# Performance work log

Hardware: AMD Instinct MI355X
Metric: run time of the kernel (lower is better)

The kernel has to match this reference:

```python
import jax, jax.numpy as jnp
import numpy as np

NU, NI, E, B, D = 100000, 50000, 1000000, 250000, 64
MSG_EPS = 1e-7   # GENConv message epsilon
BN_EPS = 1e-5    # BatchNorm1d epsilon


def setup_inputs() -> dict:
    key = jax.random.key(0)
    ks = jax.random.split(key, 8)
    x_user = jax.random.normal(ks[0], (NU, D), jnp.float32)
    x_item = jax.random.normal(ks[1], (NI, D), jnp.float32)
    src_u = jax.random.randint(ks[2], (E,), 0, NU)
    dst_i = jax.random.randint(ks[3], (E,), 0, NI)
    edge_ui = jnp.stack([src_u, dst_i]).astype(jnp.int32)   # (user, rates, item)
    pu = jax.random.randint(ks[4], (B,), 0, NU)
    pi = jax.random.randint(ks[5], (B,), 0, NI)
    pred_edge = jnp.stack([pu, pi]).astype(jnp.int32)       # supervision edges
    # per-layer (3), per-edge-type (2: 0 = user->item conv, 1 = item->user conv)
    W1 = jax.random.normal(ks[6], (3, 2, D, 2 * D), jnp.float32) / np.sqrt(D).astype(np.float32)
    b1 = jnp.zeros((3, 2, 2 * D), jnp.float32)
    gamma = jnp.ones((3, 2, 2 * D), jnp.float32)
    beta = jnp.zeros((3, 2, 2 * D), jnp.float32)
    W2 = jax.random.normal(ks[7], (3, 2, 2 * D, D), jnp.float32) / np.sqrt(2 * D).astype(np.float32)
    b2 = jnp.zeros((3, 2, D), jnp.float32)
    return dict(x_user=x_user, x_item=x_item, W1=W1, b1=b1, gamma=gamma,
                beta=beta, W2=W2, b2=b2, edge_ui=edge_ui, pred_edge=pred_edge)


def _genconv(x_src, x_dst, src_idx, dst_idx, n_dst, W1, b1, g, bt, W2, b2):
    # message: relu(x_j) + eps   (no edge attrs)
    m = jax.nn.relu(x_src[src_idx]) + MSG_EPS                     # [E, D]
    # softmax aggregation over incoming edges per destination (t = 1)
    mx = jax.ops.segment_max(m, dst_idx, num_segments=n_dst)      # [N_dst, D]
    ex = jnp.exp(m - mx[dst_idx])
    den = jax.ops.segment_sum(ex, dst_idx, num_segments=n_dst)
    w = ex / den[dst_idx]
    agg = jax.ops.segment_sum(w * m, dst_idx, num_segments=n_dst) # [N_dst, D]
    # root skip + MLP([D, 2D, D]) with BatchNorm + ReLU on hidden layer
    h = agg + x_dst
    h = h @ W1 + b1                                               # [N_dst, 2D]
    mu = h.mean(axis=0)
    var = h.var(axis=0)
    h = g * (h - mu) * jax.lax.rsqrt(var + BN_EPS) + bt
    h = jax.nn.relu(h)
    return h @ W2 + b2                                            # [N_dst, D]


def reference(x_user, x_item, W1, b1, gamma, beta, W2, b2, edge_ui, pred_edge):
    u_idx, i_idx = edge_ui[0], edge_ui[1]
    xu, xi = x_user, x_item
    for l in range(3):
        # to_hetero: one conv per edge type; aggr='sum' trivial (one edge type per dst)
        new_i = _genconv(xu, xi, u_idx, i_idx, NI,
                         W1[l, 0], b1[l, 0], gamma[l, 0], beta[l, 0], W2[l, 0], b2[l, 0])
        new_u = _genconv(xi, xu, i_idx, u_idx, NU,
                         W1[l, 1], b1[l, 1], gamma[l, 1], beta[l, 1], W2[l, 1], b2[l, 1])
        xu = jax.nn.relu(new_u)
        xi = jax.nn.relu(new_i)
    # decoder: dot product on supervision edges
    return (xu[pred_edge[0]] * xi[pred_edge[1]]).sum(axis=-1)     # [B]
```

## Files before the change

### kernel.cpp

```cpp
#include <hip/hip_runtime.h>
#include <hip/hip_fp16.h>

#define NUSR 100000
#define NITM 50000
#define NEDG 1000000
#define NPRED 250000
#define DD 64
#define DD2 128
#define MSG_EPS 1e-7f
#define BN_EPS 1e-5f
#define SCAN_B 1024

#define KI 98
#define KU 98
#define EPB 4096
#define ICAP 1536

typedef _Float16 f16x8 __attribute__((ext_vector_type(8)));
typedef float f32x4 __attribute__((ext_vector_type(4)));


__global__ __launch_bounds__(256) void count_k(
    const int* __restrict__ u_idx, const int* __restrict__ i_idx,
    int* __restrict__ deg_u, int* __restrict__ deg_i)
{
    int base = (blockIdx.x * 256 + threadIdx.x) * 4;
    int u[4], it[4];
    #pragma unroll
    for (int q = 0; q < 4; q++) {
        int e = base + q;
        u[q]  = (e < NEDG) ? u_idx[e] : -1;
        it[q] = (e < NEDG) ? i_idx[e] : -1;
    }
    #pragma unroll
    for (int q = 0; q < 4; q++) if (it[q] >= 0) atomicAdd(&deg_i[it[q]], 1);
    #pragma unroll
    for (int q = 0; q < 4; q++) if (u[q] >= 0) atomicAdd(&deg_u[u[q]], 1);
}

__global__ __launch_bounds__(SCAN_B) void scan1_k(
    const int* __restrict__ deg_i, const int* __restrict__ deg_u,
    int* __restrict__ part_i, int* __restrict__ part_u,
    int* __restrict__ bsum_i, int* __restrict__ bsum_u, int nbi)
{
    __shared__ int s[SCAN_B];
    const int* deg; int* partial; int* bsum; int n, bb;
    if ((int)blockIdx.x < nbi) { deg = deg_i; partial = part_i; bsum = bsum_i; n = NITM; bb = blockIdx.x; }
    else { deg = deg_u; partial = part_u; bsum = bsum_u; n = NUSR; bb = blockIdx.x - nbi; }
    int tid = threadIdx.x;
    int i = bb * SCAN_B + tid;
    s[tid] = (i < n) ? deg[i] : 0;
    __syncthreads();
    for (int off = 1; off < SCAN_B; off <<= 1) {
        int t = (tid >= off) ? s[tid - off] : 0;
        __syncthreads();
        s[tid] += t;
        __syncthreads();
    }
    if (i < n) partial[i] = s[tid];
    if (tid == SCAN_B - 1) bsum[bb] = s[tid];
}

__global__ __launch_bounds__(128) void scan2_k(
    int* __restrict__ bsum_i, int* __restrict__ bsum_u, int nbi, int nbu)
{
    __shared__ int s[128];
    int* bsum = (blockIdx.x == 0) ? bsum_i : bsum_u;
    int nb = (blockIdx.x == 0) ? nbi : nbu;
    int tid = threadIdx.x;
    s[tid] = (tid < nb) ? bsum[tid] : 0;
    __syncthreads();
    for (int off = 1; off < 128; off <<= 1) {
        int t = (tid >= off) ? s[tid - off] : 0;
        __syncthreads();
        s[tid] += t;
        __syncthreads();
    }
    if (tid < nb) bsum[tid] = (tid == 0) ? 0 : s[tid - 1];
}

__global__ __launch_bounds__(SCAN_B) void scan3_k(
    const int* __restrict__ deg_i, const int* __restrict__ deg_u,
    const int* __restrict__ part_i, const int* __restrict__ part_u,
    const int* __restrict__ bsum_i, const int* __restrict__ bsum_u,
    int* __restrict__ rowptr_i, int* __restrict__ rowptr_u,
    int* __restrict__ bcur_i, int* __restrict__ bcur_u, int nbi)
{
    const int* deg; const int* partial; const int* bsum;
    int* rowptr; int* bcur; int n, bb, sh;
    if ((int)blockIdx.x < nbi) {
        deg = deg_i; partial = part_i; bsum = bsum_i;
        rowptr = rowptr_i; bcur = bcur_i; n = NITM; bb = blockIdx.x; sh = 9;
    } else {
        deg = deg_u; partial = part_u; bsum = bsum_u;
        rowptr = rowptr_u; bcur = bcur_u; n = NUSR; bb = blockIdx.x - nbi; sh = 10;
    }
    int i = bb * SCAN_B + threadIdx.x;
    if (i < n) {
        int rs = partial[i] - deg[i] + bsum[bb];
        rowptr[i] = rs;
        if ((i & ((1 << sh) - 1)) == 0) bcur[i >> sh] = rs;
    }
    if (i == 0) rowptr[n] = NEDG;
}

__global__ __launch_bounds__(256) void part_k(
    const int* __restrict__ u_idx, const int* __restrict__ i_idx,
    int* __restrict__ bcur_i, int* __restrict__ bcur_u,
    int* __restrict__ pair_i, int* __restrict__ pair_u)
{
    __shared__ int lh_i[KI], lh_u[KU];
    __shared__ int lb_i[KI], lb_u[KU];
    int tid = threadIdx.x;
    int base = blockIdx.x * EPB;
    int u[16], it[16];
    #pragma unroll
    for (int q = 0; q < 16; q++) {
        int e = base + q * 256 + tid;
        u[q]  = (e < NEDG) ? u_idx[e] : -1;
        it[q] = (e < NEDG) ? i_idx[e] : -1;
    }
    if (tid < KI) lh_i[tid] = 0;
    if (tid >= 128 && tid < 128 + KU) lh_u[tid - 128] = 0;
    __syncthreads();
    #pragma unroll
    for (int q = 0; q < 16; q++) if (it[q] >= 0) {
        atomicAdd(&lh_i[it[q] >> 9], 1);
        atomicAdd(&lh_u[u[q] >> 10], 1);
    }
    __syncthreads();
    if (tid < KI) { int c = lh_i[tid]; lb_i[tid] = c ? atomicAdd(&bcur_i[tid], c) : 0; }
    if (tid >= 128 && tid < 128 + KU) {
        int k = tid - 128; int c = lh_u[k];
        lb_u[k] = c ? atomicAdd(&bcur_u[k], c) : 0;
    }
    __syncthreads();
    #pragma unroll
    for (int q = 0; q < 16; q++) if (it[q] >= 0) {
        int pi_ = atomicAdd(&lb_i[it[q] >> 9], 1);
        pair_i[pi_] = ((it[q] & 511) << 17) | u[q];
        int pu_ = atomicAdd(&lb_u[u[q] >> 10], 1);
        pair_u[pu_] = ((u[q] & 1023) << 16) | it[q];
    }
}

__global__ __launch_bounds__(1024) void bscat_k(
    const int* __restrict__ pair_i, const int* __restrict__ pair_u,
    const int* __restrict__ rowptr_i, const int* __restrict__ rowptr_u,
    int* __restrict__ csr_i, int* __restrict__ csr_u)
{
    __shared__ int cur[1024];
    int b = blockIdx.x;
    const int* pair; const int* rowptr; int* csr;
    int base_row, wrows, n, shsrc;
    if (b < KI) {
        pair = pair_i; rowptr = rowptr_i; csr = csr_i;
        base_row = b << 9; wrows = 512; n = NITM; shsrc = 17;
    } else {
        int k = b - KI;
        pair = pair_u; rowptr = rowptr_u; csr = csr_u;
        base_row = k << 10; wrows = 1024; n = NUSR; shsrc = 16;
    }
    int nrows = min(wrows, n - base_row);
    int t = threadIdx.x;
    if (t < nrows) cur[t] = rowptr[base_row + t];
    __syncthreads();
    int bstart = rowptr[base_row];
    int bend = rowptr[min(base_row + wrows, n)];
    int srcmask = (1 << shsrc) - 1;
    for (int e = bstart + t; e < bend; e += 1024) {
        int v = pair[e];
        int pos = atomicAdd(&cur[v >> shsrc], 1);
        csr[pos] = v & srcmask;
    }
}

__global__ __launch_bounds__(256) void msg0_k(
    const float* __restrict__ xu, const float* __restrict__ xi,
    __half* __restrict__ msg_u, __half* __restrict__ msg_i)
{
    int i = blockIdx.x * 256 + threadIdx.x;
    const float* x; __half* msg; int idx;
    if (i < NUSR * 16) { x = xu; msg = msg_u; idx = i; }
    else { int j = i - NUSR * 16; if (j >= NITM * 16) return; x = xi; msg = msg_i; idx = j; }
    float4 v = ((const float4*)x)[idx];
    __half2 a = __floats2half2_rn(fmaxf(v.x, 0.f) + MSG_EPS, fmaxf(v.y, 0.f) + MSG_EPS);
    __half2 b = __floats2half2_rn(fmaxf(v.z, 0.f) + MSG_EPS, fmaxf(v.w, 0.f) + MSG_EPS);
    ((__half2*)msg)[idx * 2]     = a;
    ((__half2*)msg)[idx * 2 + 1] = b;
}

__global__ __launch_bounds__(256) void wconv_k(
    const float* __restrict__ W1, const float* __restrict__ W2,
    __half* __restrict__ W1t, __half* __restrict__ W2t)
{
    int idx = blockIdx.x * 256 + threadIdx.x;
    if (idx >= 6 * 8192) return;
    int m = idx >> 13, rem = idx & 8191;
    {
        int k = rem >> 7, c = rem & 127;
        W1t[m * 8192 + c * 64 + k] = __float2half(W1[idx]);
    }
    {
        int k = rem >> 6, c = rem & 63;
        W2t[m * 8192 + c * 128 + k] = __float2half(W2[idx]);
    }
}

#define UPD4(U) { \
    float2 va=__half22float2(*(__half2*)&(U).x); \
    float2 vb=__half22float2(*(__half2*)&(U).y); \
    float2 vc=__half22float2(*(__half2*)&(U).z); \
    float2 vd=__half22float2(*(__half2*)&(U).w); \
    float e0=__expf(va.x), e1=__expf(va.y), e2=__expf(vb.x), e3=__expf(vb.y); \
    float e4=__expf(vc.x), e5=__expf(vc.y), e6=__expf(vd.x), e7=__expf(vd.y); \
    d0+=e0; n0=fmaf(e0,va.x,n0); d1+=e1; n1=fmaf(e1,va.y,n1); \
    d2+=e2; n2=fmaf(e2,vb.x,n2); d3+=e3; n3=fmaf(e3,vb.y,n3); \
    d4+=e4; n4=fmaf(e4,vc.x,n4); d5+=e5; n5=fmaf(e5,vc.y,n5); \
    d6+=e6; n6=fmaf(e6,vd.x,n6); d7+=e7; n7=fmaf(e7,vd.y,n7); }

#define GBODY(IDXE) { \
    int j = beg; \
    for (; j + 4 <= end; j += 4) { \
        int s0=(IDXE(j)), s1=(IDXE(j+1)), s2=(IDXE(j+2)), s3=(IDXE(j+3)); \
        uint4 u0 = mp4[s0*8+l8]; uint4 u1 = mp4[s1*8+l8]; \
        uint4 u2 = mp4[s2*8+l8]; uint4 u3 = mp4[s3*8+l8]; \
        UPD4(u0) UPD4(u1) UPD4(u2) UPD4(u3) } \
    for (; j < end; j++) { int ss=(IDXE(j)); uint4 uu = mp4[ss*8+l8]; UPD4(uu) } }

#define IDX_L(jj) su.idx[(jj)]
#define IDX_G(jj) csr[blkBeg + (jj)]

union AggSU { int idx[ICAP]; float red[8][128]; };

__global__ __launch_bounds__(256) void aggemm1f_k(
    const __half* __restrict__ msg_i_src, const __half* __restrict__ msg_u_src,
    const float* __restrict__ xi_cur, const float* __restrict__ xu_cur,
    const int* __restrict__ rowptr_i, const int* __restrict__ rowptr_u,
    const int* __restrict__ csr_i, const int* __restrict__ csr_u,
    const __half* __restrict__ W1t_l,
    const float* __restrict__ b1_l,
    __half* __restrict__ h1_i, __half* __restrict__ h1_u,
    double* __restrict__ gs_l,
    int gI)
{
    __shared__ _Float16 sA[64][88];
    __shared__ AggSU su;

    int side = ((int)blockIdx.x < gI) ? 0 : 1;
    int bb = side ? (blockIdx.x - gI) : blockIdx.x;
    const __half* msg = side ? msg_i_src : msg_u_src;
    const float* xdst = side ? xu_cur : xi_cur;
    const int* rowptr = side ? rowptr_u : rowptr_i;
    const int* csr    = side ? csr_u : csr_i;
    const __half* W1t = W1t_l + (size_t)side * 8192;
    const float* b1   = b1_l + side * DD2;
    __half* h1        = side ? h1_u : h1_i;
    double* gsum      = gs_l + side * 256;
    double* gsq       = gsum + 128;
    int N             = side ? NUSR : NITM;

    int t = threadIdx.x;
    int r0 = bb * 64;
    int w = t >> 6, lane = t & 63;
    int g = lane >> 3, l8 = lane & 7;
    int q = lane >> 4, ln = lane & 15;
    const uint4* mp4 = (const uint4*)msg;

    int blkBeg = rowptr[r0];
    int blkEnd = rowptr[min(r0 + 64, N)];
    int nE = blkEnd - blkBeg;
    for (int e = t; e < nE && e < ICAP; e += 256) su.idx[e] = csr[blkBeg + e];
    __syncthreads();

    #pragma unroll
    for (int ii = 0; ii < 2; ii++) {
        int rr = w * 16 + ii * 8 + g;
        int r = r0 + rr;
        uint4 o = make_uint4(0u, 0u, 0u, 0u);
        if (r < N) {
            int beg = rowptr[r] - blkBeg;
            int end = rowptr[r + 1] - blkBeg;
            float d0=0.f,d1=0.f,d2=0.f,d3=0.f,d4=0.f,d5=0.f,d6=0.f,d7=0.f;
            float n0=0.f,n1=0.f,n2=0.f,n3=0.f,n4=0.f,n5=0.f,n6=0.f,n7=0.f;
            if (end <= ICAP) { GBODY(IDX_L) } else { GBODY(IDX_G) }
            bool nz = end > beg;
            float a0 = nz ? n0/d0 : 0.f, a1 = nz ? n1/d1 : 0.f;
            float a2 = nz ? n2/d2 : 0.f, a3 = nz ? n3/d3 : 0.f;
            float a4 = nz ? n4/d4 : 0.f, a5 = nz ? n5/d5 : 0.f;
            float a6 = nz ? n6/d6 : 0.f, a7 = nz ? n7/d7 : 0.f;
            const float4* xr = (const float4*)xdst + (size_t)r * 16;
            float4 x0 = xr[l8 * 2], x1 = xr[l8 * 2 + 1];
            __half2 p0 = __floats2half2_rn(a0 + x0.x, a1 + x0.y);
            __half2 p1 = __floats2half2_rn(a2 + x0.z, a3 + x0.w);
            __half2 p2 = __floats2half2_rn(a4 + x1.x, a5 + x1.y);
            __half2 p3 = __floats2half2_rn(a6 + x1.z, a7 + x1.w);
            o.x = *(unsigned int*)&p0; o.y = *(unsigned int*)&p1;
            o.z = *(unsigned int*)&p2; o.w = *(unsigned int*)&p3;
        }
        *(uint4*)&sA[rr][l8 * 8] = o;
    }
    __syncthreads();

    f16x8 afr[4][2], bfr[2][2];
    #pragma unroll
    for (int rt = 0; rt < 4; rt++)
        #pragma unroll
        for (int ks = 0; ks < 2; ks++)
            afr[rt][ks] = *(const f16x8*)&sA[rt * 16 + ln][ks * 32 + q * 8];
    const f16x8* Wv = (const f16x8*)W1t;
    #pragma unroll
    for (int ct = 0; ct < 2; ct++)
        #pragma unroll
        for (int ks = 0; ks < 2; ks++)
            bfr[ct][ks] = Wv[(w * 32 + ct * 16 + ln) * 8 + ks * 4 + q];

    f32x4 acc[4][2];
    #pragma unroll
    for (int rt = 0; rt < 4; rt++)
        #pragma unroll
        for (int ct = 0; ct < 2; ct++)
            acc[rt][ct] = (f32x4){0.f, 0.f, 0.f, 0.f};

    #pragma unroll
    for (int rt = 0; rt < 4; rt++)
        #pragma unroll
        for (int ct = 0; ct < 2; ct++) {
            acc[rt][ct] = __builtin_amdgcn_mfma_f32_16x16x32_f16(
                afr[rt][0], bfr[ct][0], acc[rt][ct], 0, 0, 0);
            acc[rt][ct] = __builtin_amdgcn_mfma_f32_16x16x32_f16(
                afr[rt][1], bfr[ct][1], acc[rt][ct], 0, 0, 0);
        }

    float b1c0 = b1[w * 32 + ln];
    float b1c1 = b1[w * 32 + 16 + ln];
    float ps0 = 0.f, pq0 = 0.f, ps1 = 0.f, pq1 = 0.f;
    #pragma unroll
    for (int rt = 0; rt < 4; rt++) {
        #pragma unroll
        for (int i = 0; i < 4; i++) {
            int r = r0 + rt * 16 + q * 4 + i;
            if (r < N) {
                float h0 = acc[rt][0][i] + b1c0;
                float h1v = acc[rt][1][i] + b1c1;
                h1[(size_t)r * DD2 + w * 32 + ln] = __float2half(h0);
                h1[(size_t)r * DD2 + w * 32 + 16 + ln] = __float2half(h1v);
                ps0 += h0; pq0 += h0 * h0;
                ps1 += h1v; pq1 += h1v * h1v;
            }
        }
    }
    su.red[q][w * 32 + ln] = ps0;      su.red[q][w * 32 + 16 + ln] = ps1;
    su.red[4 + q][w * 32 + ln] = pq0;  su.red[4 + q][w * 32 + 16 + ln] = pq1;
    __syncthreads();
    if (t < 128) {
        float s = 0.f, qq = 0.f;
        #pragma unroll
        for (int k = 0; k < 4; k++) { s += su.red[k][t]; qq += su.red[4 + k][t]; }
        atomicAdd(&gsum[t], (double)s);
        atomicAdd(&gsq[t],  (double)qq);
    }
}

__global__ __launch_bounds__(256) void gemm2f_k(
    const __half* __restrict__ h1_i, const __half* __restrict__ h1_u,
    const double* __restrict__ gs_l,
    const float* __restrict__ gamma_l, const float* __restrict__ beta_l,
    const __half* __restrict__ W2t_l, const float* __restrict__ b2_l,
    float* __restrict__ xi_new, float* __restrict__ xu_new,
    __half* __restrict__ msgi_out, __half* __restrict__ msgu_out, int gI)
{
    __shared__ _Float16 sA[64][136];
    __shared__ float2 sss[DD2];

    int side = ((int)blockIdx.x < gI) ? 0 : 1;
    int bb = side ? (blockIdx.x - gI) : blockIdx.x;
    const __half* h1   = side ? h1_u : h1_i;
    const double* gsum = gs_l + side * 256;
    const double* gsq  = gsum + 128;
    const float* gamma = gamma_l + side * DD2;
    const float* beta  = beta_l + side * DD2;
    const __half* W2t  = W2t_l + (size_t)side * 8192;
    const float* b2    = b2_l + side * DD;
    float* xnew        = side ? xu_new : xi_new;
    __half* msgout     = side ? msgu_out : msgi_out;
    int N              = side ? NUSR : NITM;

    int t = threadIdx.x;
    if (t < 128) {
        double mean = gsum[t] / (double)N;
        double var  = gsq[t] / (double)N - mean * mean;
        float inv = (float)(1.0 / sqrt(var + (double)BN_EPS));
        float sc = gamma[t] * inv;
        sss[t] = make_float2(sc, beta[t] - (float)mean * sc);
    }
    __syncthreads();

    int r0 = bb * 64;
    for (int i = t; i < 2048; i += 256) {
        int rr = i >> 5, c4 = i & 31;
        int r = r0 + rr;
        uint2 o = make_uint2(0u, 0u);
        if (r < N) {
            uint2 hv = ((const uint2*)h1)[(size_t)r * 32 + c4];
            float2 va = __half22float2(*(__half2*)&hv.x);
            float2 vb = __half22float2(*(__half2*)&hv.y);
            float2 s0 = sss[c4 * 4], s1 = sss[c4 * 4 + 1];
            float2 s2 = sss[c4 * 4 + 2], s3 = sss[c4 * 4 + 3];
            va.x = fmaxf(fmaf(va.x, s0.x, s0.y), 0.f);
            va.y = fmaxf(fmaf(va.y, s1.x, s1.y), 0.f);
            vb.x = fmaxf(fmaf(vb.x, s2.x, s2.y), 0.f);
            vb.y = fmaxf(fmaf(vb.y, s3.x, s3.y), 0.f);
            __half2 a = __floats2half2_rn(va.x, va.y);
            __half2 b = __floats2half2_rn(vb.x, vb.y);
            o.x = *(unsigned int*)&a; o.y = *(unsigned int*)&b;
        }
        *(uint2*)&sA[rr][c4 * 4] = o;
    }
    __syncthreads();

    int w = t >> 6, lane = t & 63, q = lane >> 4, ln = lane & 15;
    f32x4 acc[4];
    #pragma unroll
    for (int rt = 0; rt < 4; rt++) acc[rt] = (f32x4){0.f, 0.f, 0.f, 0.f};

    const f16x8* Wv = (const f16x8*)W2t;
    #pragma unroll
    for (int ks = 0; ks < 4; ks++) {
        f16x8 bf = Wv[(w * 16 + ln) * 16 + ks * 4 + q];
        #pragma unroll
        for (int rt = 0; rt < 4; rt++) {
            f16x8 af = *(const f16x8*)&sA[rt * 16 + ln][ks * 32 + q * 8];
            acc[rt] = __builtin_amdgcn_mfma_f32_16x16x32_f16(af, bf, acc[rt], 0, 0, 0);
        }
    }

    int c = w * 16 + ln;
    float bb2 = b2[c];
    #pragma unroll
    for (int rt = 0; rt < 4; rt++) {
        #pragma unroll
        for (int i = 0; i < 4; i++) {
            int r = r0 + rt * 16 + q * 4 + i;
            if (r < N) {
                float o = fmaxf(acc[rt][i] + bb2, 0.f);
                xnew[(size_t)r * DD + c] = o;
                msgout[(size_t)r * DD + c] = __float2half(o + MSG_EPS);
            }
        }
    }
}

__global__ __launch_bounds__(256) void decode_k(
    const float* __restrict__ xu, const float* __restrict__ xi,
    const int* __restrict__ pu, const int* __restrict__ pi,
    float* __restrict__ out)
{
    int idx = blockIdx.x * 256 + threadIdx.x;
    int b = idx >> 4, lane = idx & 15;
    if (b >= NPRED) return;
    int u = pu[b], it = pi[b];
    float4 a = ((const float4*)(xu + (size_t)u * DD))[lane];
    float4 c = ((const float4*)(xi + (size_t)it * DD))[lane];
    float s = a.x * c.x + a.y * c.y + a.z * c.z + a.w * c.w;
    #pragma unroll
    for (int off = 8; off; off >>= 1) s += __shfl_down(s, off, 16);
    if (lane == 0) out[b] = s;
}

extern "C" void kernel_launch(void* const* d_in, const int* in_sizes, int n_in,
                              void* d_out, int out_size, void* d_ws, size_t ws_size,
                              hipStream_t stream)
{
    const float* x_user = (const float*)d_in[0];
    const float* x_item = (const float*)d_in[1];
    const float* W1    = (const float*)d_in[2];
    const float* b1    = (const float*)d_in[3];
    const float* gamma = (const float*)d_in[4];
    const float* beta  = (const float*)d_in[5];
    const float* W2    = (const float*)d_in[6];
    const float* b2    = (const float*)d_in[7];
    const int* edge = (const int*)d_in[8];
    const int* pred = (const int*)d_in[9];
    float* out = (float*)d_out;

    const int* u_idx = edge;
    const int* i_idx = edge + NEDG;

    char* p = (char*)d_ws;
    #define ALLOC(ptr, type, count) \
        type* ptr = (type*)p; p += (((size_t)(count) * sizeof(type)) + 255) & ~(size_t)255;

    ALLOC(deg_i, int, NITM)
    ALLOC(deg_u, int, NUSR)
    ALLOC(gsumAll, double, 12 * 256)
    size_t zero_span = (char*)p - (char*)deg_i;
    ALLOC(part_i, int, NITM)
    ALLOC(part_u, int, NUSR)
    ALLOC(bsum_i, int, 128)
    ALLOC(bsum_u, int, 128)
    ALLOC(bcur_i, int, 128)
    ALLOC(bcur_u, int, 128)
    ALLOC(rowptr_i, int, NITM + 1)
    ALLOC(rowptr_u, int, NUSR + 1)
    ALLOC(csr_i, int, NEDG)
    ALLOC(csr_u, int, NEDG)
    ALLOC(h1_i, __half, (size_t)NITM * DD2)
    ALLOC(h1_u, __half, (size_t)NUSR * DD2)
    ALLOC(W1t, __half, 6 * 8192)
    ALLOC(W2t, __half, 6 * 8192)
    ALLOC(xu0, float, (size_t)NUSR * DD)
    ALLOC(xu1, float, (size_t)NUSR * DD)
    ALLOC(xi0, float, (size_t)NITM * DD)
    ALLOC(xi1, float, (size_t)NITM * DD)
    ALLOC(msg_u, __half, (size_t)NUSR * DD)
    ALLOC(msg_i0, __half, (size_t)NITM * DD)
    ALLOC(msg_i1, __half, (size_t)NITM * DD)
    #undef ALLOC
    float* xu_buf[2] = {xu0, xu1};
    float* xi_buf[2] = {xi0, xi1};

    int* pair_i = (int*)h1_i;
    int* pair_u = (int*)h1_u;

    hipMemsetAsync(deg_i, 0, zero_span, stream);
    int eb4 = (NEDG / 4 + 255) / 256;
    count_k<<<eb4, 256, 0, stream>>>(u_idx, i_idx, deg_u, deg_i);

    int nbi = (NITM + SCAN_B - 1) / SCAN_B;
    int nbu = (NUSR + SCAN_B - 1) / SCAN_B;
    scan1_k<<<nbi + nbu, SCAN_B, 0, stream>>>(deg_i, deg_u, part_i, part_u,
                                              bsum_i, bsum_u, nbi);
    scan2_k<<<2, 128, 0, stream>>>(bsum_i, bsum_u, nbi, nbu);
    scan3_k<<<nbi + nbu, SCAN_B, 0, stream>>>(deg_i, deg_u, part_i, part_u,
                                              bsum_i, bsum_u, rowptr_i, rowptr_u,
                                              bcur_i, bcur_u, nbi);
    int pb = (NEDG + EPB - 1) / EPB;
    part_k<<<pb, 256, 0, stream>>>(u_idx, i_idx, bcur_i, bcur_u, pair_i, pair_u);
    bscat_k<<<KI + KU, 1024, 0, stream>>>(pair_i, pair_u, rowptr_i, rowptr_u,
                                          csr_i, csr_u);

    wconv_k<<<(6 * 8192 + 255) / 256, 256, 0, stream>>>(W1, W2, W1t, W2t);
    msg0_k<<<((NUSR + NITM) * 16 + 255) / 256, 256, 0, stream>>>(x_user, x_item,
                                                                 msg_u, msg_i0);

    int gI = (NITM + 63) / 64;
    int gU = (NUSR + 63) / 64;
    const float* cu = x_user;
    const float* ci = x_item;
    __half* msgi = msg_i0;
    __half* msgi_alt = msg_i1;
    for (int l = 0; l < 3; l++) {
        float* ni = xi_buf[l & 1];
        float* nu = xu_buf[l & 1];
        aggemm1f_k<<<gI + gU, 256, 0, stream>>>(
            msgi, msg_u, ci, cu, rowptr_i, rowptr_u, csr_i, csr_u,
            W1t + (size_t)l * 2 * 8192, b1 + (size_t)l * 2 * DD2,
            h1_i, h1_u, gsumAll + l * 2 * 256, gI);
        gemm2f_k<<<gI + gU, 256, 0, stream>>>(
            h1_i, h1_u, gsumAll + l * 2 * 256,
            gamma + (size_t)l * 2 * DD2, beta + (size_t)l * 2 * DD2,
            W2t + (size_t)l * 2 * 8192, b2 + (size_t)l * 2 * DD,
            ni, nu, msgi_alt, msg_u, gI);
        cu = nu; ci = ni;
        __half* tmp = msgi; msgi = msgi_alt; msgi_alt = tmp;
    }

    decode_k<<<(NPRED * 16) / 256, 256, 0, stream>>>(cu, ci, pred, pred + NPRED, out);
}
```

Before: 568.7 us.

## Store activations as fp16, pre-scale messages by log2e, use raw v_exp_f32

Messages are now stored pre-multiplied by log2(e), so the gather loop can call the hardware v_exp_f32 instruction directly instead of __expf, and the aggregate is scaled back by ln2. Between layers the node features are kept only as fp16 copies, which the first GEMM reads instead of fp32. Only the final layer writes fp32 features for the decoder. This cuts exp instruction count and memory traffic for the intermediate features, at the cost of extra fp16 rounding of the root-skip term and of the scaled messages.

```diff
diff --git a/kernel.cpp b/kernel.cpp
--- a/kernel.cpp
+++ b/kernel.cpp
@@ -10,6 +10,8 @@
 #define MSG_EPS 1e-7f
 #define BN_EPS 1e-5f
 #define SCAN_B 1024
+#define LOG2E 1.44269504088896340736f
+#define LN2F 0.69314718055994530942f
 
 #define KI 98
 #define KU 98
@@ -19,6 +21,10 @@
 typedef _Float16 f16x8 __attribute__((ext_vector_type(8)));
 typedef float f32x4 __attribute__((ext_vector_type(4)));
 
+
+__device__ __forceinline__ float exp2a(float x) {
+    float r; asm("v_exp_f32 %0, %1" : "=v"(r) : "v"(x)); return r;
+}
 
 __global__ __launch_bounds__(256) void count_k(
     const int* __restrict__ u_idx, const int* __restrict__ i_idx,
@@ -177,17 +183,25 @@
 
 __global__ __launch_bounds__(256) void msg0_k(
     const float* __restrict__ xu, const float* __restrict__ xi,
-    __half* __restrict__ msg_u, __half* __restrict__ msg_i)
+    __half* __restrict__ ef_u, __half* __restrict__ ef_i,
+    __half* __restrict__ xh_u, __half* __restrict__ xh_i)
 {
     int i = blockIdx.x * 256 + threadIdx.x;
-    const float* x; __half* msg; int idx;
-    if (i < NUSR * 16) { x = xu; msg = msg_u; idx = i; }
-    else { int j = i - NUSR * 16; if (j >= NITM * 16) return; x = xi; msg = msg_i; idx = j; }
+    const float* x; __half* ef; __half* xh; int idx;
+    if (i < NUSR * 16) { x = xu; ef = ef_u; xh = xh_u; idx = i; }
+    else { int j = i - NUSR * 16; if (j >= NITM * 16) return; x = xi; ef = ef_i; xh = xh_i; idx = j; }
     float4 v = ((const float4*)x)[idx];
-    __half2 a = __floats2half2_rn(fmaxf(v.x, 0.f) + MSG_EPS, fmaxf(v.y, 0.f) + MSG_EPS);
-    __half2 b = __floats2half2_rn(fmaxf(v.z, 0.f) + MSG_EPS, fmaxf(v.w, 0.f) + MSG_EPS);
-    ((__half2*)msg)[idx * 2]     = a;
-    ((__half2*)msg)[idx * 2 + 1] = b;
+    float m0 = (fmaxf(v.x, 0.f) + MSG_EPS) * LOG2E;
+    float m1 = (fmaxf(v.y, 0.f) + MSG_EPS) * LOG2E;
+    float m2 = (fmaxf(v.z, 0.f) + MSG_EPS) * LOG2E;
+    float m3 = (fmaxf(v.w, 0.f) + MSG_EPS) * LOG2E;
+    __half2 e01 = __floats2half2_rn(m0, m1), e23 = __floats2half2_rn(m2, m3);
+    __half2 x01 = __floats2half2_rn(v.x, v.y), x23 = __floats2half2_rn(v.z, v.w);
+    uint2 ew, xw;
+    ew.x = *(unsigned int*)&e01; ew.y = *(unsigned int*)&e23;
+    xw.x = *(unsigned int*)&x01; xw.y = *(unsigned int*)&x23;
+    ((uint2*)ef)[idx] = ew;
+    ((uint2*)xh)[idx] = xw;
 }
 
 __global__ __launch_bounds__(256) void wconv_k(
@@ -212,8 +226,8 @@
     float2 vb=__half22float2(*(__half2*)&(U).y); \
     float2 vc=__half22float2(*(__half2*)&(U).z); \
     float2 vd=__half22float2(*(__half2*)&(U).w); \
-    float e0=__expf(va.x), e1=__expf(va.y), e2=__expf(vb.x), e3=__expf(vb.y); \
-    float e4=__expf(vc.x), e5=__expf(vc.y), e6=__expf(vd.x), e7=__expf(vd.y); \
+    float e0=exp2a(va.x), e1=exp2a(va.y), e2=exp2a(vb.x), e3=exp2a(vb.y); \
+    float e4=exp2a(vc.x), e5=exp2a(vc.y), e6=exp2a(vd.x), e7=exp2a(vd.y); \
     d0+=e0; n0=fmaf(e0,va.x,n0); d1+=e1; n1=fmaf(e1,va.y,n1); \
     d2+=e2; n2=fmaf(e2,vb.x,n2); d3+=e3; n3=fmaf(e3,vb.y,n3); \
     d4+=e4; n4=fmaf(e4,vc.x,n4); d5+=e5; n5=fmaf(e5,vc.y,n5); \
@@ -223,10 +237,10 @@
     int j = beg; \
     for (; j + 4 <= end; j += 4) { \
         int s0=(IDXE(j)), s1=(IDXE(j+1)), s2=(IDXE(j+2)), s3=(IDXE(j+3)); \
-        uint4 u0 = mp4[s0*8+l8]; uint4 u1 = mp4[s1*8+l8]; \
-        uint4 u2 = mp4[s2*8+l8]; uint4 u3 = mp4[s3*8+l8]; \
+        uint4 u0 = mp4[(size_t)s0*8+l8]; uint4 u1 = mp4[(size_t)s1*8+l8]; \
+        uint4 u2 = mp4[(size_t)s2*8+l8]; uint4 u3 = mp4[(size_t)s3*8+l8]; \
         UPD4(u0) UPD4(u1) UPD4(u2) UPD4(u3) } \
-    for (; j < end; j++) { int ss=(IDXE(j)); uint4 uu = mp4[ss*8+l8]; UPD4(uu) } }
+    for (; j < end; j++) { int ss=(IDXE(j)); uint4 uu = mp4[(size_t)ss*8+l8]; UPD4(uu) } }
 
 #define IDX_L(jj) su.idx[(jj)]
 #define IDX_G(jj) csr[blkBeg + (jj)]
@@ -234,8 +248,8 @@
 union AggSU { int idx[ICAP]; float red[8][128]; };
 
 __global__ __launch_bounds__(256) void aggemm1f_k(
-    const __half* __restrict__ msg_i_src, const __half* __restrict__ msg_u_src,
-    const float* __restrict__ xi_cur, const float* __restrict__ xu_cur,
+    const __half* __restrict__ ef_i_src, const __half* __restrict__ ef_u_src,
+    const __half* __restrict__ xhi_cur, const __half* __restrict__ xhu_cur,
     const int* __restrict__ rowptr_i, const int* __restrict__ rowptr_u,
     const int* __restrict__ csr_i, const int* __restrict__ csr_u,
     const __half* __restrict__ W1t_l,
@@ -249,8 +263,8 @@
 
     int side = ((int)blockIdx.x < gI) ? 0 : 1;
     int bb = side ? (blockIdx.x - gI) : blockIdx.x;
-    const __half* msg = side ? msg_i_src : msg_u_src;
-    const float* xdst = side ? xu_cur : xi_cur;
+    const __half* ef  = side ? ef_i_src : ef_u_src;
+    const __half* xh  = side ? xhu_cur : xhi_cur;
     const int* rowptr = side ? rowptr_u : rowptr_i;
     const int* csr    = side ? csr_u : csr_i;
     const __half* W1t = W1t_l + (size_t)side * 8192;
@@ -265,7 +279,7 @@
     int w = t >> 6, lane = t & 63;
     int g = lane >> 3, l8 = lane & 7;
     int q = lane >> 4, ln = lane & 15;
-    const uint4* mp4 = (const uint4*)msg;
+    const uint4* mp4 = (const uint4*)ef;
 
     int blkBeg = rowptr[r0];
     int blkEnd = rowptr[min(r0 + 64, N)];
@@ -285,16 +299,19 @@
             float n0=0.f,n1=0.f,n2=0.f,n3=0.f,n4=0.f,n5=0.f,n6=0.f,n7=0.f;
             if (end <= ICAP) { GBODY(IDX_L) } else { GBODY(IDX_G) }
             bool nz = end > beg;
-            float a0 = nz ? n0/d0 : 0.f, a1 = nz ? n1/d1 : 0.f;
-            float a2 = nz ? n2/d2 : 0.f, a3 = nz ? n3/d3 : 0.f;
-            float a4 = nz ? n4/d4 : 0.f, a5 = nz ? n5/d5 : 0.f;
-            float a6 = nz ? n6/d6 : 0.f, a7 = nz ? n7/d7 : 0.f;
-            const float4* xr = (const float4*)xdst + (size_t)r * 16;
-            float4 x0 = xr[l8 * 2], x1 = xr[l8 * 2 + 1];
-            __half2 p0 = __floats2half2_rn(a0 + x0.x, a1 + x0.y);
-            __half2 p1 = __floats2half2_rn(a2 + x0.z, a3 + x0.w);
-            __half2 p2 = __floats2half2_rn(a4 + x1.x, a5 + x1.y);
-            __half2 p3 = __floats2half2_rn(a6 + x1.z, a7 + x1.w);
+            float a0 = nz ? (n0/d0)*LN2F : 0.f, a1 = nz ? (n1/d1)*LN2F : 0.f;
+            float a2 = nz ? (n2/d2)*LN2F : 0.f, a3 = nz ? (n3/d3)*LN2F : 0.f;
+            float a4 = nz ? (n4/d4)*LN2F : 0.f, a5 = nz ? (n5/d5)*LN2F : 0.f;
+            float a6 = nz ? (n6/d6)*LN2F : 0.f, a7 = nz ? (n7/d7)*LN2F : 0.f;
+            uint4 xv = ((const uint4*)xh)[(size_t)r * 8 + l8];
+            float2 x01 = __half22float2(*(__half2*)&xv.x);
+            float2 x23 = __half22float2(*(__half2*)&xv.y);
+            float2 x45 = __half22float2(*(__half2*)&xv.z);
+            float2 x67 = __half22float2(*(__half2*)&xv.w);
+            __half2 p0 = __floats2half2_rn(a0 + x01.x, a1 + x01.y);
+            __half2 p1 = __floats2half2_rn(a2 + x23.x, a3 + x23.y);
+            __half2 p2 = __floats2half2_rn(a4 + x45.x, a5 + x45.y);
+            __half2 p3 = __floats2half2_rn(a6 + x67.x, a7 + x67.y);
             o.x = *(unsigned int*)&p0; o.y = *(unsigned int*)&p1;
             o.z = *(unsigned int*)&p2; o.w = *(unsigned int*)&p3;
         }
@@ -368,7 +385,9 @@
     const float* __restrict__ gamma_l, const float* __restrict__ beta_l,
     const __half* __restrict__ W2t_l, const float* __restrict__ b2_l,
     float* __restrict__ xi_new, float* __restrict__ xu_new,
-    __half* __restrict__ msgi_out, __half* __restrict__ msgu_out, int gI)
+    __half* __restrict__ xhi_out, __half* __restrict__ xhu_out,
+    __half* __restrict__ efi_out, __half* __restrict__ efu_out,
+    int last, int gI)
 {
     __shared__ _Float16 sA[64][136];
     __shared__ float2 sss[DD2];
@@ -383,7 +402,8 @@
     const __half* W2t  = W2t_l + (size_t)side * 8192;
     const float* b2    = b2_l + side * DD;
     float* xnew        = side ? xu_new : xi_new;
-    __half* msgout     = side ? msgu_out : msgi_out;
+    __half* xhout      = side ? xhu_out : xhi_out;
+    __half* efout      = side ? efu_out : efi_out;
     int N              = side ? NUSR : NITM;
 
     int t = threadIdx.x;
@@ -444,8 +464,12 @@
             int r = r0 + rt * 16 + q * 4 + i;
             if (r < N) {
                 float o = fmaxf(acc[rt][i] + bb2, 0.f);
-                xnew[(size_t)r * DD + c] = o;
-                msgout[(size_t)r * DD + c] = __float2half(o + MSG_EPS);
+                if (last) {
+                    xnew[(size_t)r * DD + c] = o;
+                } else {
+                    xhout[(size_t)r * DD + c] = __float2half(o);
+                    efout[(size_t)r * DD + c] = __float2half((o + MSG_EPS) * LOG2E);
+                }
             }
         }
     }
@@ -509,16 +533,16 @@
     ALLOC(h1_u, __half, (size_t)NUSR * DD2)
     ALLOC(W1t, __half, 6 * 8192)
     ALLOC(W2t, __half, 6 * 8192)
-    ALLOC(xu0, float, (size_t)NUSR * DD)
-    ALLOC(xu1, float, (size_t)NUSR * DD)
-    ALLOC(xi0, float, (size_t)NITM * DD)
-    ALLOC(xi1, float, (size_t)NITM * DD)
-    ALLOC(msg_u, __half, (size_t)NUSR * DD)
-    ALLOC(msg_i0, __half, (size_t)NITM * DD)
-    ALLOC(msg_i1, __half, (size_t)NITM * DD)
+    ALLOC(xu_f, float, (size_t)NUSR * DD)
+    ALLOC(xi_f, float, (size_t)NITM * DD)
+    ALLOC(xh_u0, __half, (size_t)NUSR * DD)
+    ALLOC(xh_u1, __half, (size_t)NUSR * DD)
+    ALLOC(xh_i0, __half, (size_t)NITM * DD)
+    ALLOC(xh_i1, __half, (size_t)NITM * DD)
+    ALLOC(ef_u, __half, (size_t)NUSR * DD)
+    ALLOC(ef_i0, __half, (size_t)NITM * DD)
+    ALLOC(ef_i1, __half, (size_t)NITM * DD)
     #undef ALLOC
-    float* xu_buf[2] = {xu0, xu1};
-    float* xi_buf[2] = {xi0, xi1};
 
     int* pair_i = (int*)h1_i;
     int* pair_u = (int*)h1_u;
@@ -541,30 +565,29 @@
                                           csr_i, csr_u);
 
     wconv_k<<<(6 * 8192 + 255) / 256, 256, 0, stream>>>(W1, W2, W1t, W2t);
-    msg0_k<<<((NUSR + NITM) * 16 + 255) / 256, 256, 0, stream>>>(x_user, x_item,
-                                                                 msg_u, msg_i0);
+    msg0_k<<<((NUSR + NITM) * 16 + 255) / 256, 256, 0, stream>>>(
+        x_user, x_item, ef_u, ef_i0, xh_u0, xh_i0);
 
     int gI = (NITM + 63) / 64;
     int gU = (NUSR + 63) / 64;
-    const float* cu = x_user;
-    const float* ci = x_item;
-    __half* msgi = msg_i0;
-    __half* msgi_alt = msg_i1;
+    __half* efi = ef_i0;
+    __half* efi_alt = ef_i1;
     for (int l = 0; l < 3; l++) {
-        float* ni = xi_buf[l & 1];
-        float* nu = xu_buf[l & 1];
+        const __half* xhi_c = (l & 1) ? xh_i1 : xh_i0;
+        const __half* xhu_c = (l & 1) ? xh_u1 : xh_u0;
+        __half* xhi_o = (l & 1) ? xh_i0 : xh_i1;
+        __half* xhu_o = (l & 1) ? xh_u0 : xh_u1;
         aggemm1f_k<<<gI + gU, 256, 0, stream>>>(
-            msgi, msg_u, ci, cu, rowptr_i, rowptr_u, csr_i, csr_u,
+            efi, ef_u, xhi_c, xhu_c, rowptr_i, rowptr_u, csr_i, csr_u,
             W1t + (size_t)l * 2 * 8192, b1 + (size_t)l * 2 * DD2,
             h1_i, h1_u, gsumAll + l * 2 * 256, gI);
         gemm2f_k<<<gI + gU, 256, 0, stream>>>(
             h1_i, h1_u, gsumAll + l * 2 * 256,
             gamma + (size_t)l * 2 * DD2, beta + (size_t)l * 2 * DD2,
             W2t + (size_t)l * 2 * 8192, b2 + (size_t)l * 2 * DD,
-            ni, nu, msgi_alt, msg_u, gI);
-        cu = nu; ci = ni;
-        __half* tmp = msgi; msgi = msgi_alt; msgi_alt = tmp;
-    }
-
-    decode_k<<<(NPRED * 16) / 256, 256, 0, stream>>>(cu, ci, pred, pred + NPRED, out);
-}
+            xi_f, xu_f, xhi_o, xhu_o, efi_alt, ef_u, (l == 2) ? 1 : 0, gI);
+        __half* tmp = efi; efi = efi_alt; efi_alt = tmp;
+    }
+
+    decode_k<<<(NPRED * 16) / 256, 256, 0, stream>>>(xu_f, xi_f, pred, pred + NPRED, out);
+}
```

Result: no change. 570.0 us (+0.2%).
